# Performance work log

Hardware: AMD Instinct MI355X
Metric: run time of the kernel (lower is better)

The kernel has to match this reference:

```python
import jax, jax.numpy as jnp
import numpy as np

ALPHA = 0.2  # LeakyReLU slope
NEG_INF = -9e15


def setup_inputs() -> dict:
    key = jax.random.key(0)
    ks = jax.random.split(key, 10)
    N, K, d = 20000, 32, 128
    R, S = 100, 4  # num relations, num domains
    item_embs = jax.random.normal(ks[0], (N, d), dtype=jnp.float32)
    entity_embs = jax.random.normal(ks[1], (N, K, d), dtype=jnp.float32)
    relations_embed = jax.random.normal(ks[2], (N, K, d), dtype=jnp.float32)
    relation_ids = jax.random.randint(ks[3], (N, K), 0, R, dtype=jnp.int32)
    adj_mask = jax.random.randint(ks[4], (N, K), 0, 2, dtype=jnp.int32)
    # fc_attention: Linear(3d, 1); out: Linear(d, d)
    fc_w = jax.random.normal(ks[5], (1, 3 * d), dtype=jnp.float32) * (1.0 / np.sqrt(3 * d))
    fc_b = jnp.zeros((1,), dtype=jnp.float32)
    out_w = jax.random.normal(ks[6], (d, d), dtype=jnp.float32) * (1.0 / np.sqrt(d))
    out_b = jnp.zeros((d,), dtype=jnp.float32)
    rel_dom_probs = jax.nn.softmax(jax.random.normal(ks[7], (R, S), dtype=jnp.float32), axis=-1)
    return {"item_embs": item_embs, "entity_embs": entity_embs,
            "relations_embed": relations_embed, "relation_ids": relation_ids,
            "adj_mask": adj_mask, "fc_w": fc_w, "fc_b": fc_b,
            "out_w": out_w, "out_b": out_b, "rel_dom_probs": rel_dom_probs}


def reference(item_embs, entity_embs, relations_embed, relation_ids, adj_mask,
              fc_w, fc_b, out_w, out_b, rel_dom_probs):
    N, K, d = entity_embs.shape
    R = rel_dom_probs.shape[0]
    # edge attention score: Linear(3d,1) on [item | relation | entity], then LeakyReLU
    Wh = jnp.broadcast_to(item_embs[:, None, :], (N, K, d))
    att_in = jnp.concatenate([Wh, relations_embed, entity_embs], axis=-1)  # [N,K,3d]
    e = jnp.einsum('nkf,of->nk', att_in, fc_w) + fc_b[0]
    e = jnp.where(e > 0, e, ALPHA * e)
    # masked softmax over neighbors (dropout inert in eval)
    masked = jnp.where(adj_mask > 0, e, NEG_INF)
    pi = jax.nn.softmax(masked, axis=1)  # [N,K]
    base = pi[..., None] * relations_embed * entity_embs  # [N,K,d]
    # domain-weighted aggregation: sum_s probs[rel_id, s], invalid ids -> 0
    valid = (relation_ids >= 0) & (relation_ids < R)
    safe_ids = jnp.clip(relation_ids, 0, R - 1)
    a_total = jnp.where(valid, rel_dom_probs[safe_ids].sum(-1), 0.0)  # [N,K]
    agg = jnp.einsum('nk,nkd->nd', a_total, base)  # [N,d]
    # residual + output Linear + ReLU
    out = (agg + item_embs) @ out_w.T + out_b
    return jax.nn.relu(out)
```

## Files before the change

### kernel.cpp

```cpp
#include <hip/hip_runtime.h>

#define ALPHA 0.2f

__device__ __forceinline__ float dot4(float4 a, float4 b) {
    return a.x * b.x + a.y * b.y + a.z * b.z + a.w * b.w;
}

__device__ __forceinline__ void lds_fence() {
    asm volatile("s_waitcnt lgkmcnt(0)" ::: "memory");
    __builtin_amdgcn_sched_barrier(0);
}

__device__ __forceinline__ void async16(const float* g, float* l) {
    __builtin_amdgcn_global_load_lds(
        (const __attribute__((address_space(1))) void*)g,
        (__attribute__((address_space(3))) void*)l, 16, 0, 0);
}

__global__ __launch_bounds__(64, 1)
void gat_k1(const float* __restrict__ item,
            const float* __restrict__ ent,
            const float* __restrict__ rel,
            const int*   __restrict__ rel_ids,
            const int*   __restrict__ adj,
            const float* __restrict__ fc_w,
            const float* __restrict__ fc_b,
            const float* __restrict__ probs,
            float* __restrict__ y,
            int N, int R)
{
    __shared__ __align__(16) float slab[8192];
    __shared__ float strip[32];
    __shared__ float asum[128];

    const int l  = threadIdx.x;
    const int lh = l & 31;
    const int hi = l >> 5;

    for (int i = l; i < R; i += 64) {
        float4 q = *(const float4*)&probs[i * 4];
        asum[i] = q.x + q.y + q.z + q.w;
    }
    const float4 fi = *(const float4*)&fc_w[4 * lh];
    const float4 fr = *(const float4*)&fc_w[128 + 4 * lh];
    const float4 fe = *(const float4*)&fc_w[256 + 4 * lh];
    const float  fcb = fc_b[0];
    lds_fence();

    for (int n = blockIdx.x; n < N; n += gridDim.x) {
        const float4 item4 = *(const float4*)&item[(size_t)n * 128 + 4 * lh];
        const int adjv = adj[(size_t)n * 32 + lh];
        const int idv  = rel_ids[(size_t)n * 32 + lh];

        const float* bR = rel + (size_t)n * 4096 + 4 * l;
        const float* bE = ent + (size_t)n * 4096 + 4 * l;
        #pragma unroll
        for (int c = 0; c < 16; ++c) {
            async16(bR + c * 256, &slab[c * 256]);
            async16(bE + c * 256, &slab[4096 + c * 256]);
        }

        float ep[16];
#define ECHUNK(c, imm) \
        asm volatile("s_waitcnt vmcnt(" imm ")" ::: "memory"); \
        __builtin_amdgcn_sched_barrier(0); \
        { float4 rv = *(const float4*)&slab[(c) * 256 + 4 * l]; \
          float4 ev = *(const float4*)&slab[4096 + (c) * 256 + 4 * l]; \
          ep[(c)] = dot4(rv, fr) + dot4(ev, fe); }
        ECHUNK(0, "28")  ECHUNK(1, "26")  ECHUNK(2, "24")  ECHUNK(3, "22")
        ECHUNK(4, "20")  ECHUNK(5, "18")  ECHUNK(6, "16")  ECHUNK(7, "14")
        ECHUNK(8, "12")  ECHUNK(9, "10")  ECHUNK(10, "8")  ECHUNK(11, "6")
        ECHUNK(12, "4")  ECHUNK(13, "2")  ECHUNK(14, "0")  ECHUNK(15, "0")
#undef ECHUNK

        float sit = dot4(item4, fi);
        #pragma unroll
        for (int s = 16; s >= 1; s >>= 1) sit += __shfl_xor(sit, s, 32);

        #pragma unroll
        for (int c = 0; c < 16; ++c) {
            float v = ep[c];
            #pragma unroll
            for (int s = 16; s >= 1; s >>= 1) v += __shfl_xor(v, s, 32);
            ep[c] = v;
        }
        if (lh == 0) {
            #pragma unroll
            for (int c = 0; c < 16; ++c) strip[2 * c + hi] = ep[c];
        }
        lds_fence();

        float e = strip[lh] + sit + fcb;
        e = (e > 0.0f) ? e : ALPHA * e;
        float ex = (adjv > 0) ? __expf(e) : 0.0f;
        float Z = ex;
        #pragma unroll
        for (int s = 16; s >= 1; s >>= 1) Z += __shfl_xor(Z, s, 32);
        const bool  vld = (idv >= 0) && (idv < R);
        const float a   = vld ? asum[idv] : 0.0f;
        const float wk  = (Z > 0.0f) ? (ex * a / Z) : (a * (1.0f / 32.0f));

        float4 acc = make_float4(0.f, 0.f, 0.f, 0.f);
        #pragma unroll
        for (int c = 0; c < 16; ++c) {
            const float wc = __shfl(wk, 2 * c + hi, 64);
            const float4 rv = *(const float4*)&slab[c * 256 + 4 * l];
            const float4 ev = *(const float4*)&slab[4096 + c * 256 + 4 * l];
            acc.x = fmaf(wc, rv.x * ev.x, acc.x);
            acc.y = fmaf(wc, rv.y * ev.y, acc.y);
            acc.z = fmaf(wc, rv.z * ev.z, acc.z);
            acc.w = fmaf(wc, rv.w * ev.w, acc.w);
        }
        acc.x += __shfl_xor(acc.x, 32, 64);
        acc.y += __shfl_xor(acc.y, 32, 64);
        acc.z += __shfl_xor(acc.z, 32, 64);
        acc.w += __shfl_xor(acc.w, 32, 64);

        if (l < 32) {
            float4 o;
            o.x = acc.x + item4.x;
            o.y = acc.y + item4.y;
            o.z = acc.z + item4.z;
            o.w = acc.w + item4.w;
            *(float4*)&y[(size_t)n * 128 + 4 * lh] = o;
        }
    }
}

__device__ __forceinline__ void block_bar() {
    asm volatile("s_waitcnt lgkmcnt(0)" ::: "memory");
    __builtin_amdgcn_s_barrier();
}

__global__ __launch_bounds__(256, 4)
void gat_k2(const float* __restrict__ out_w,
            const float* __restrict__ out_b,
            float* __restrict__ y, int N)
{
    __shared__ __align__(16) float ylds[128];
    __shared__ __align__(16) float plds[1024];

    const int t = threadIdx.x;
    const int c = t & 7;
    const int g = t >> 3;

    float4 w4[16];
    #pragma unroll
    for (int a = 0; a < 4; ++a)
        #pragma unroll
        for (int i = 0; i < 4; ++i)
            w4[a * 4 + i] = *(const float4*)&out_w[(size_t)(g * 4 + a) * 128 + c * 16 + i * 4];
    const float bj = out_b[t & 127];
    const int stride = gridDim.x;

    float vcur = 0.0f;
    if (t < 128) vcur = y[(size_t)blockIdx.x * 128 + t];

    for (int n = blockIdx.x; n < N; n += stride) {
        if (t < 128) ylds[t] = vcur;
        block_bar();
        int np = n + stride; if (np >= N) np = n;
        float vn = 0.0f;
        if (t < 128) vn = y[(size_t)np * 128 + t];

        float4 yc[4];
        #pragma unroll
        for (int i = 0; i < 4; ++i) yc[i] = *(const float4*)&ylds[c * 16 + i * 4];
        #pragma unroll
        for (int a = 0; a < 4; ++a) {
            float s = 0.0f;
            #pragma unroll
            for (int i = 0; i < 4; ++i) s += dot4(w4[a * 4 + i], yc[i]);
            plds[a * 256 + g * 8 + c] = s;
        }
        block_bar();
        if (t < 128) {
            const int j = t, a2 = j & 3, g2 = j >> 2;
            const float* pp = &plds[a2 * 256 + g2 * 8];
            float4 u0 = *(const float4*)pp;
            float4 u1 = *(const float4*)(pp + 4);
            float s = u0.x + u0.y + u0.z + u0.w + u1.x + u1.y + u1.z + u1.w + bj;
            y[(size_t)n * 128 + j] = fmaxf(s, 0.0f);
        }
        vcur = vn;
    }
}

extern "C" void kernel_launch(void* const* d_in, const int* in_sizes, int n_in,
                              void* d_out, int out_size, void* d_ws, size_t ws_size,
                              hipStream_t stream) {
    const float* item    = (const float*)d_in[0];
    const float* ent     = (const float*)d_in[1];
    const float* rel     = (const float*)d_in[2];
    const int*   rel_ids = (const int*)  d_in[3];
    const int*   adj     = (const int*)  d_in[4];
    const float* fc_w    = (const float*)d_in[5];
    const float* fc_b    = (const float*)d_in[6];
    const float* out_w   = (const float*)d_in[7];
    const float* out_b   = (const float*)d_in[8];
    const float* probs   = (const float*)d_in[9];
    float* out = (float*)d_out;

    const int N = in_sizes[0] / 128;
    const int R = in_sizes[9] / 4;

    hipLaunchKernelGGL(gat_k1, dim3(1024), dim3(64), 0, stream,
                       item, ent, rel, rel_ids, adj, fc_w, fc_b, probs, out, N, R);

    int blocks2 = 2048; if (blocks2 > N) blocks2 = N;
    hipLaunchKernelGGL(gat_k2, dim3(blocks2), dim3(256), 0, stream,
                       out_w, out_b, out, N);
}
```

Measured before the change: 159.1 us.

## Double-buffer neighbor slabs in LDS with register prefetch of the next node

The attention/aggregation kernel now software-pipelines across nodes. While it computes node n, it issues async global-to-LDS loads for node n+grid into a second LDS buffer and loads the last 4 chunks plus the item, adj and id values into registers. This is meant to hide the global load latency that each node previously waited on in full. The LDS slab grows to 48KB and register pressure rises, and the grid is cut from 1024 to 768 blocks, which changes occupancy and load balance.

Result: no change. 160.6 us (+0.9%).

```diff
diff --git a/kernel.cpp b/kernel.cpp
--- a/kernel.cpp
+++ b/kernel.cpp
@@ -16,6 +16,97 @@
         (const __attribute__((address_space(1))) void*)g,
         (__attribute__((address_space(3))) void*)l, 16, 0, 0);
 }
+
+#define VMW(imm) do { \
+    asm volatile("s_waitcnt vmcnt(" imm ")" ::: "memory"); \
+    __builtin_amdgcn_sched_barrier(0); } while (0)
+
+#define ECH(c, imm) \
+    VMW(imm); \
+    { float4 rv = *(const float4*)(sp + (c) * 512 + 4 * l); \
+      float4 ev = *(const float4*)(sp + (c) * 512 + 256 + 4 * l); \
+      ep[c] = dot4(rv, fr) + dot4(ev, fe); }
+
+#define ITER(NCUR, SPOFF, SQOFF, RcR, RcE, RnR, RnE, ScIT, ScADJ, ScID, SnIT, SnADJ, SnID) do { \
+    const float* sp = &slab[SPOFF]; \
+    float ep[16]; \
+    ECH(0, "31")  ECH(1, "29")  ECH(2, "27")  ECH(3, "25") \
+    ECH(4, "23")  ECH(5, "21")  ECH(6, "19")  ECH(7, "17") \
+    ECH(8, "15")  ECH(9, "13")  ECH(10, "11") ECH(11, "9") \
+    _Pragma("unroll") \
+    for (int c = 0; c < 4; ++c) \
+        ep[12 + c] = dot4(RcR[c], fr) + dot4(RcE[c], fe); \
+    {  \
+      int np = (NCUR) + GS; if (np >= N) np = n0; \
+      const float* bR = rel + (size_t)np * 4096 + 4 * l; \
+      const float* bE = ent + (size_t)np * 4096 + 4 * l; \
+      float* sq = &slab[SQOFF]; \
+      lds_fence(); \
+      _Pragma("unroll") \
+      for (int c = 0; c < 12; ++c) { \
+          async16(bR + c * 256, sq + c * 512); \
+          async16(bE + c * 256, sq + c * 512 + 256); } \
+      __builtin_amdgcn_sched_barrier(0);  \
+      _Pragma("unroll") \
+      for (int c = 0; c < 4; ++c) { \
+          RnR[c] = *(const float4*)(bR + (12 + c) * 256); \
+          RnE[c] = *(const float4*)(bE + (12 + c) * 256); } \
+      SnIT  = *(const float4*)&item[(size_t)np * 128 + 4 * lh]; \
+      SnADJ = adj[(size_t)np * 32 + lh]; \
+      SnID  = rel_ids[(size_t)np * 32 + lh]; \
+    } \
+     \
+    float sit = dot4(ScIT, fi); \
+    _Pragma("unroll") \
+    for (int s = 16; s >= 1; s >>= 1) sit += __shfl_xor(sit, s, 32); \
+    _Pragma("unroll") \
+    for (int c = 0; c < 16; ++c) { \
+        float v = ep[c]; \
+        _Pragma("unroll") \
+        for (int s = 16; s >= 1; s >>= 1) v += __shfl_xor(v, s, 32); \
+        ep[c] = v; } \
+    if (lh == 0) { \
+        _Pragma("unroll") \
+        for (int c = 0; c < 16; ++c) strip[2 * c + hi] = ep[c]; } \
+    lds_fence(); \
+     \
+    float e = strip[lh] + sit + fcb; \
+    e = (e > 0.0f) ? e : ALPHA * e; \
+    float ex = (ScADJ > 0) ? __expf(e) : 0.0f; \
+    float Z = ex; \
+    _Pragma("unroll") \
+    for (int s = 16; s >= 1; s >>= 1) Z += __shfl_xor(Z, s, 32); \
+    const bool vld = (ScID >= 0) && (ScID < R); \
+    const float av = vld ? asum[ScID] : 0.0f; \
+    const float wk = (Z > 0.0f) ? (ex * av / Z) : (av * (1.0f / 32.0f)); \
+     \
+    float4 acc = make_float4(0.f, 0.f, 0.f, 0.f); \
+    _Pragma("unroll") \
+    for (int c = 0; c < 12; ++c) { \
+        const float wc = __shfl(wk, 2 * c + hi, 64); \
+        float4 rv = *(const float4*)(sp + c * 512 + 4 * l); \
+        float4 ev = *(const float4*)(sp + c * 512 + 256 + 4 * l); \
+        acc.x = fmaf(wc, rv.x * ev.x, acc.x); \
+        acc.y = fmaf(wc, rv.y * ev.y, acc.y); \
+        acc.z = fmaf(wc, rv.z * ev.z, acc.z); \
+        acc.w = fmaf(wc, rv.w * ev.w, acc.w); } \
+    _Pragma("unroll") \
+    for (int c = 0; c < 4; ++c) { \
+        const float wc = __shfl(wk, 2 * (12 + c) + hi, 64); \
+        acc.x = fmaf(wc, RcR[c].x * RcE[c].x, acc.x); \
+        acc.y = fmaf(wc, RcR[c].y * RcE[c].y, acc.y); \
+        acc.z = fmaf(wc, RcR[c].z * RcE[c].z, acc.z); \
+        acc.w = fmaf(wc, RcR[c].w * RcE[c].w, acc.w); } \
+    acc.x += __shfl_xor(acc.x, 32, 64); \
+    acc.y += __shfl_xor(acc.y, 32, 64); \
+    acc.z += __shfl_xor(acc.z, 32, 64); \
+    acc.w += __shfl_xor(acc.w, 32, 64); \
+    if (l < 32) { \
+        float4 o; \
+        o.x = acc.x + ScIT.x; o.y = acc.y + ScIT.y; \
+        o.z = acc.z + ScIT.z; o.w = acc.w + ScIT.w; \
+        *(float4*)&y[(size_t)(NCUR) * 128 + 4 * lh] = o; } \
+} while (0)
 
 __global__ __launch_bounds__(64, 1)
 void gat_k1(const float* __restrict__ item,
@@ -29,7 +120,7 @@
             float* __restrict__ y,
             int N, int R)
 {
-    __shared__ __align__(16) float slab[8192];
+    __shared__ __align__(16) float slab[12288];
     __shared__ float strip[32];
     __shared__ float asum[128];
 
@@ -44,86 +135,41 @@
     const float4 fi = *(const float4*)&fc_w[4 * lh];
     const float4 fr = *(const float4*)&fc_w[128 + 4 * lh];
     const float4 fe = *(const float4*)&fc_w[256 + 4 * lh];
-    const float  fcb = fc_b[0];
+    const float fcb = fc_b[0];
     lds_fence();
 
-    for (int n = blockIdx.x; n < N; n += gridDim.x) {
-        const float4 item4 = *(const float4*)&item[(size_t)n * 128 + 4 * lh];
-        const int adjv = adj[(size_t)n * 32 + lh];
-        const int idv  = rel_ids[(size_t)n * 32 + lh];
-
-        const float* bR = rel + (size_t)n * 4096 + 4 * l;
-        const float* bE = ent + (size_t)n * 4096 + 4 * l;
-        #pragma unroll
-        for (int c = 0; c < 16; ++c) {
-            async16(bR + c * 256, &slab[c * 256]);
-            async16(bE + c * 256, &slab[4096 + c * 256]);
-        }
-
-        float ep[16];
-#define ECHUNK(c, imm) \
-        asm volatile("s_waitcnt vmcnt(" imm ")" ::: "memory"); \
-        __builtin_amdgcn_sched_barrier(0); \
-        { float4 rv = *(const float4*)&slab[(c) * 256 + 4 * l]; \
-          float4 ev = *(const float4*)&slab[4096 + (c) * 256 + 4 * l]; \
-          ep[(c)] = dot4(rv, fr) + dot4(ev, fe); }
-        ECHUNK(0, "28")  ECHUNK(1, "26")  ECHUNK(2, "24")  ECHUNK(3, "22")
-        ECHUNK(4, "20")  ECHUNK(5, "18")  ECHUNK(6, "16")  ECHUNK(7, "14")
-        ECHUNK(8, "12")  ECHUNK(9, "10")  ECHUNK(10, "8")  ECHUNK(11, "6")
-        ECHUNK(12, "4")  ECHUNK(13, "2")  ECHUNK(14, "0")  ECHUNK(15, "0")
-#undef ECHUNK
-
-        float sit = dot4(item4, fi);
-        #pragma unroll
-        for (int s = 16; s >= 1; s >>= 1) sit += __shfl_xor(sit, s, 32);
-
-        #pragma unroll
-        for (int c = 0; c < 16; ++c) {
-            float v = ep[c];
-            #pragma unroll
-            for (int s = 16; s >= 1; s >>= 1) v += __shfl_xor(v, s, 32);
-            ep[c] = v;
-        }
-        if (lh == 0) {
-            #pragma unroll
-            for (int c = 0; c < 16; ++c) strip[2 * c + hi] = ep[c];
-        }
-        lds_fence();
-
-        float e = strip[lh] + sit + fcb;
-        e = (e > 0.0f) ? e : ALPHA * e;
-        float ex = (adjv > 0) ? __expf(e) : 0.0f;
-        float Z = ex;
-        #pragma unroll
-        for (int s = 16; s >= 1; s >>= 1) Z += __shfl_xor(Z, s, 32);
-        const bool  vld = (idv >= 0) && (idv < R);
-        const float a   = vld ? asum[idv] : 0.0f;
-        const float wk  = (Z > 0.0f) ? (ex * a / Z) : (a * (1.0f / 32.0f));
-
-        float4 acc = make_float4(0.f, 0.f, 0.f, 0.f);
-        #pragma unroll
-        for (int c = 0; c < 16; ++c) {
-            const float wc = __shfl(wk, 2 * c + hi, 64);
-            const float4 rv = *(const float4*)&slab[c * 256 + 4 * l];
-            const float4 ev = *(const float4*)&slab[4096 + c * 256 + 4 * l];
-            acc.x = fmaf(wc, rv.x * ev.x, acc.x);
-            acc.y = fmaf(wc, rv.y * ev.y, acc.y);
-            acc.z = fmaf(wc, rv.z * ev.z, acc.z);
-            acc.w = fmaf(wc, rv.w * ev.w, acc.w);
-        }
-        acc.x += __shfl_xor(acc.x, 32, 64);
-        acc.y += __shfl_xor(acc.y, 32, 64);
-        acc.z += __shfl_xor(acc.z, 32, 64);
-        acc.w += __shfl_xor(acc.w, 32, 64);
-
-        if (l < 32) {
-            float4 o;
-            o.x = acc.x + item4.x;
-            o.y = acc.y + item4.y;
-            o.z = acc.z + item4.z;
-            o.w = acc.w + item4.w;
-            *(float4*)&y[(size_t)n * 128 + 4 * lh] = o;
-        }
+    const int GS = gridDim.x;
+    const int n0 = blockIdx.x;
+
+    float4 rA[4], eA[4], rB[4], eB[4];
+    float4 itA, itB;
+    int adjA = 0, idA = 0, adjB = 0, idB = 0;
+
+    {
+        const float* bR = rel + (size_t)n0 * 4096 + 4 * l;
+        const float* bE = ent + (size_t)n0 * 4096 + 4 * l;
+        #pragma unroll
+        for (int c = 0; c < 12; ++c) {
+            async16(bR + c * 256, &slab[c * 512]);
+            async16(bE + c * 256, &slab[c * 512 + 256]);
+        }
+        __builtin_amdgcn_sched_barrier(0);
+        #pragma unroll
+        for (int c = 0; c < 4; ++c) {
+            rA[c] = *(const float4*)(bR + (12 + c) * 256);
+            eA[c] = *(const float4*)(bE + (12 + c) * 256);
+        }
+        itA  = *(const float4*)&item[(size_t)n0 * 128 + 4 * lh];
+        adjA = adj[(size_t)n0 * 32 + lh];
+        idA  = rel_ids[(size_t)n0 * 32 + lh];
+    }
+
+    int n = n0;
+    while (true) {
+        ITER(n, 0, 6144, rA, eA, rB, eB, itA, adjA, idA, itB, adjB, idB);
+        n += GS; if (n >= N) break;
+        ITER(n, 6144, 0, rB, eB, rA, eA, itB, adjB, idB, itA, adjA, idA);
+        n += GS; if (n >= N) break;
     }
 }
 
@@ -204,7 +250,7 @@
     const int N = in_sizes[0] / 128;
     const int R = in_sizes[9] / 4;
 
-    hipLaunchKernelGGL(gat_k1, dim3(1024), dim3(64), 0, stream,
+    hipLaunchKernelGGL(gat_k1, dim3(768), dim3(64), 0, stream,
                        item, ent, rel, rel_ids, adj, fc_w, fc_b, probs, out, N, R);
 
     int blocks2 = 2048; if (blocks2 > N) blocks2 = N;
```

## Split each node across four waves with register-prefetched neighbor rows

Applied to the files above, without the earlier changes.

The first kernel now uses 256-thread blocks where each wave handles eight of the 32 neighbors. Each thread keeps the relation and entity rows in registers and prefetches the next node's data in the previous iteration, replacing the single-wave LDS slab filled with async global-to-LDS loads. Partial aggregates are combined across waves through shared memory with two block barriers per node. The aim is more memory-level parallelism and occupancy for this bandwidth-bound stage, at the cost of extra barriers and cross-wave reduction.

Result: no change. 159.8 us (+0.4%).

```diff
diff --git a/kernel.cpp b/kernel.cpp
--- a/kernel.cpp
+++ b/kernel.cpp
@@ -6,18 +6,12 @@
     return a.x * b.x + a.y * b.y + a.z * b.z + a.w * b.w;
 }
 
-__device__ __forceinline__ void lds_fence() {
+__device__ __forceinline__ void block_bar() {
     asm volatile("s_waitcnt lgkmcnt(0)" ::: "memory");
-    __builtin_amdgcn_sched_barrier(0);
-}
-
-__device__ __forceinline__ void async16(const float* g, float* l) {
-    __builtin_amdgcn_global_load_lds(
-        (const __attribute__((address_space(1))) void*)g,
-        (__attribute__((address_space(3))) void*)l, 16, 0, 0);
-}
-
-__global__ __launch_bounds__(64, 1)
+    __builtin_amdgcn_s_barrier();
+}
+
+__global__ __launch_bounds__(256, 4)
 void gat_k1(const float* __restrict__ item,
             const float* __restrict__ ent,
             const float* __restrict__ rel,
@@ -29,107 +23,129 @@
             float* __restrict__ y,
             int N, int R)
 {
-    __shared__ __align__(16) float slab[8192];
-    __shared__ float strip[32];
+    __shared__ float e_lds[32];
+    __shared__ __align__(16) float part[4][128];
     __shared__ float asum[128];
 
-    const int l  = threadIdx.x;
+    const int t  = threadIdx.x;
+    const int w  = t >> 6;
+    const int l  = t & 63;
     const int lh = l & 31;
     const int hi = l >> 5;
-
-    for (int i = l; i < R; i += 64) {
+    const int kb = w * 8;
+
+    for (int i = t; i < R; i += 256) {
         float4 q = *(const float4*)&probs[i * 4];
         asum[i] = q.x + q.y + q.z + q.w;
     }
     const float4 fi = *(const float4*)&fc_w[4 * lh];
     const float4 fr = *(const float4*)&fc_w[128 + 4 * lh];
     const float4 fe = *(const float4*)&fc_w[256 + 4 * lh];
-    const float  fcb = fc_b[0];
-    lds_fence();
-
-    for (int n = blockIdx.x; n < N; n += gridDim.x) {
-        const float4 item4 = *(const float4*)&item[(size_t)n * 128 + 4 * lh];
-        const int adjv = adj[(size_t)n * 32 + lh];
-        const int idv  = rel_ids[(size_t)n * 32 + lh];
-
-        const float* bR = rel + (size_t)n * 4096 + 4 * l;
-        const float* bE = ent + (size_t)n * 4096 + 4 * l;
-        #pragma unroll
-        for (int c = 0; c < 16; ++c) {
-            async16(bR + c * 256, &slab[c * 256]);
-            async16(bE + c * 256, &slab[4096 + c * 256]);
-        }
-
-        float ep[16];
-#define ECHUNK(c, imm) \
-        asm volatile("s_waitcnt vmcnt(" imm ")" ::: "memory"); \
-        __builtin_amdgcn_sched_barrier(0); \
-        { float4 rv = *(const float4*)&slab[(c) * 256 + 4 * l]; \
-          float4 ev = *(const float4*)&slab[4096 + (c) * 256 + 4 * l]; \
-          ep[(c)] = dot4(rv, fr) + dot4(ev, fe); }
-        ECHUNK(0, "28")  ECHUNK(1, "26")  ECHUNK(2, "24")  ECHUNK(3, "22")
-        ECHUNK(4, "20")  ECHUNK(5, "18")  ECHUNK(6, "16")  ECHUNK(7, "14")
-        ECHUNK(8, "12")  ECHUNK(9, "10")  ECHUNK(10, "8")  ECHUNK(11, "6")
-        ECHUNK(12, "4")  ECHUNK(13, "2")  ECHUNK(14, "0")  ECHUNK(15, "0")
-#undef ECHUNK
-
-        float sit = dot4(item4, fi);
+    const float fcb = fc_b[0];
+    __syncthreads();
+
+    const int ST = gridDim.x;
+    const int n0 = blockIdx.x;
+
+    float4 rc[4], ec[4], itc;
+    int adjc, idc;
+    {
+        const float* bR = rel + (size_t)n0 * 4096;
+        const float* bE = ent + (size_t)n0 * 4096;
+        #pragma unroll
+        for (int c = 0; c < 4; ++c) {
+            const int kk = kb + 2 * c + hi;
+            rc[c] = *(const float4*)&bR[kk * 128 + 4 * lh];
+            ec[c] = *(const float4*)&bE[kk * 128 + 4 * lh];
+        }
+        itc  = *(const float4*)&item[(size_t)n0 * 128 + 4 * lh];
+        adjc = adj[(size_t)n0 * 32 + lh];
+        idc  = rel_ids[(size_t)n0 * 32 + lh];
+    }
+
+    for (int n = n0; n < N; n += ST) {
+        float4 p[4];
+        float  ep[4];
+        #pragma unroll
+        for (int c = 0; c < 4; ++c) {
+            p[c].x = rc[c].x * ec[c].x;
+            p[c].y = rc[c].y * ec[c].y;
+            p[c].z = rc[c].z * ec[c].z;
+            p[c].w = rc[c].w * ec[c].w;
+            ep[c]  = dot4(rc[c], fr) + dot4(ec[c], fe);
+        }
+        float sit = dot4(itc, fi);
+        const float4 it_cur = itc;
+        const int adj_cur = adjc, id_cur = idc;
+
+        int np = n + ST; if (np >= N) np = n0;
+        {
+            const float* bR = rel + (size_t)np * 4096;
+            const float* bE = ent + (size_t)np * 4096;
+            #pragma unroll
+            for (int c = 0; c < 4; ++c) {
+                const int kk = kb + 2 * c + hi;
+                rc[c] = *(const float4*)&bR[kk * 128 + 4 * lh];
+                ec[c] = *(const float4*)&bE[kk * 128 + 4 * lh];
+            }
+            itc  = *(const float4*)&item[(size_t)np * 128 + 4 * lh];
+            adjc = adj[(size_t)np * 32 + lh];
+            idc  = rel_ids[(size_t)np * 32 + lh];
+        }
+
         #pragma unroll
         for (int s = 16; s >= 1; s >>= 1) sit += __shfl_xor(sit, s, 32);
-
-        #pragma unroll
-        for (int c = 0; c < 16; ++c) {
+        #pragma unroll
+        for (int c = 0; c < 4; ++c) {
             float v = ep[c];
             #pragma unroll
             for (int s = 16; s >= 1; s >>= 1) v += __shfl_xor(v, s, 32);
             ep[c] = v;
         }
-        if (lh == 0) {
-            #pragma unroll
-            for (int c = 0; c < 16; ++c) strip[2 * c + hi] = ep[c];
-        }
-        lds_fence();
-
-        float e = strip[lh] + sit + fcb;
+        #pragma unroll
+        for (int c = 0; c < 4; ++c)
+            if (lh == c) e_lds[kb + 2 * c + hi] = ep[c];
+        block_bar();
+
+        float e = e_lds[lh] + sit + fcb;
         e = (e > 0.0f) ? e : ALPHA * e;
-        float ex = (adjv > 0) ? __expf(e) : 0.0f;
+        float ex = (adj_cur > 0) ? __expf(e) : 0.0f;
         float Z = ex;
         #pragma unroll
         for (int s = 16; s >= 1; s >>= 1) Z += __shfl_xor(Z, s, 32);
-        const bool  vld = (idv >= 0) && (idv < R);
-        const float a   = vld ? asum[idv] : 0.0f;
+        const bool  vld = (id_cur >= 0) && (id_cur < R);
+        const float a   = vld ? asum[vld ? id_cur : 0] : 0.0f;
         const float wk  = (Z > 0.0f) ? (ex * a / Z) : (a * (1.0f / 32.0f));
 
         float4 acc = make_float4(0.f, 0.f, 0.f, 0.f);
         #pragma unroll
-        for (int c = 0; c < 16; ++c) {
-            const float wc = __shfl(wk, 2 * c + hi, 64);
-            const float4 rv = *(const float4*)&slab[c * 256 + 4 * l];
-            const float4 ev = *(const float4*)&slab[4096 + c * 256 + 4 * l];
-            acc.x = fmaf(wc, rv.x * ev.x, acc.x);
-            acc.y = fmaf(wc, rv.y * ev.y, acc.y);
-            acc.z = fmaf(wc, rv.z * ev.z, acc.z);
-            acc.w = fmaf(wc, rv.w * ev.w, acc.w);
+        for (int c = 0; c < 4; ++c) {
+            const float wc = __shfl(wk, kb + 2 * c + hi, 32);
+            acc.x = fmaf(wc, p[c].x, acc.x);
+            acc.y = fmaf(wc, p[c].y, acc.y);
+            acc.z = fmaf(wc, p[c].z, acc.z);
+            acc.w = fmaf(wc, p[c].w, acc.w);
         }
         acc.x += __shfl_xor(acc.x, 32, 64);
         acc.y += __shfl_xor(acc.y, 32, 64);
         acc.z += __shfl_xor(acc.z, 32, 64);
         acc.w += __shfl_xor(acc.w, 32, 64);
-
-        if (l < 32) {
+        if (hi == 0) *(float4*)&part[w][4 * lh] = acc;
+        block_bar();
+
+        if (t < 32) {
+            const float4 a0 = *(const float4*)&part[0][4 * t];
+            const float4 a1 = *(const float4*)&part[1][4 * t];
+            const float4 a2 = *(const float4*)&part[2][4 * t];
+            const float4 a3 = *(const float4*)&part[3][4 * t];
             float4 o;
-            o.x = acc.x + item4.x;
-            o.y = acc.y + item4.y;
-            o.z = acc.z + item4.z;
-            o.w = acc.w + item4.w;
-            *(float4*)&y[(size_t)n * 128 + 4 * lh] = o;
-        }
-    }
-}
-
-__device__ __forceinline__ void block_bar() {
-    asm volatile("s_waitcnt lgkmcnt(0)" ::: "memory");
-    __builtin_amdgcn_s_barrier();
+            o.x = a0.x + a1.x + a2.x + a3.x + it_cur.x;
+            o.y = a0.y + a1.y + a2.y + a3.y + it_cur.y;
+            o.z = a0.z + a1.z + a2.z + a3.z + it_cur.z;
+            o.w = a0.w + a1.w + a2.w + a3.w + it_cur.w;
+            *(float4*)&y[(size_t)n * 128 + 4 * t] = o;
+        }
+    }
 }
 
 __global__ __launch_bounds__(256, 4)
@@ -204,7 +220,7 @@
     const int N = in_sizes[0] / 128;
     const int R = in_sizes[9] / 4;
 
-    hipLaunchKernelGGL(gat_k1, dim3(1024), dim3(64), 0, stream,
+    hipLaunchKernelGGL(gat_k1, dim3(2000), dim3(256), 0, stream,
                        item, ent, rel, rel_ids, adj, fc_w, fc_b, probs, out, N, R);
 
     int blocks2 = 2048; if (blocks2 > N) blocks2 = N;
```
